# Kernel tuning notes

Measured on AMD Instinct MI355X. Metric: run time of the kernel, lower is better.

The kernel has to match this reference:

```python
import jax, jax.numpy as jnp
import numpy as np

N, DIM, DK, DV = 8192, 512, 128, 512


def setup_inputs() -> dict:
    key = jax.random.key(0)
    ks = jax.random.split(key, 6)
    return {
        "x": jax.random.normal(ks[0], (N, DIM), dtype=jnp.float32),
        "w_w": jax.random.normal(ks[1], (DK, DIM), dtype=jnp.float32) * (1.0 / np.sqrt(DIM)),
        "w_b": jax.random.normal(ks[2], (DK,), dtype=jnp.float32) * 0.01,
        "wv_w": jax.random.normal(ks[3], (DV, DIM), dtype=jnp.float32) * (1.0 / np.sqrt(DIM)),
        "wv_b": jax.random.normal(ks[4], (DV,), dtype=jnp.float32) * 0.01,
        "a": jax.random.normal(ks[5], (2 * DK,), dtype=jnp.float32),
    }


def reference(x, w_w, w_b, wv_w, wv_b, a):
    dk = w_b.shape[0]
    # eqx.nn.Linear: y = W @ x + b, applied per-row via vmap -> x @ W.T + b
    wx = x @ w_w.T + w_b                       # [n, dk]
    e_src = wx @ a[:dk]                        # [n], sum(wx_i * a1)
    e_dst = wx @ a[dk:]                        # [n], sum(wx_j * a2)
    logits = jax.nn.leaky_relu(e_src[:, None] + e_dst[None, :])  # [n, n]
    score = jax.nn.softmax(logits, axis=-1)    # row-wise softmax
    v = x @ wv_w.T + wv_b                      # [n, dv]
    return score @ v                           # [n, dv]
```

## Files before the change

### kernel.cpp

```cpp
#include <hip/hip_runtime.h>
#include <hip/hip_bf16.h>

#define N_   8192
#define DIM_ 512
#define DK_  128
#define DV_  512
#define L2E_ 1.44269504088896f
#define NCH_ 512
#define CHR_ 16

typedef short short8 __attribute__((ext_vector_type(8)));
typedef float f32x4  __attribute__((ext_vector_type(4)));

__device__ __forceinline__ float fexp2(float x) { return __builtin_amdgcn_exp2f(x); }

__device__ __forceinline__ ushort f2bf(float f) {
    union { float f; unsigned u; } v; v.f = f;
    unsigned u = v.u;
    return (ushort)((u + 0x7FFFu + ((u >> 16) & 1u)) >> 16);
}
__device__ __forceinline__ float bf2f(ushort u) { return __uint_as_float(((unsigned)u) << 16); }
__device__ __forceinline__ float decode_max(unsigned u) {
    return __uint_as_float((u & 0x80000000u) ? (u ^ 0x80000000u) : ~u);
}

__global__ __launch_bounds__(256) void prep_kernel(const float* __restrict__ w_w,
                            const float* __restrict__ w_b, const float* __restrict__ a,
                            const float* __restrict__ wv_w,
                            float* __restrict__ u1, float* __restrict__ u2,
                            float* __restrict__ scal, ushort* __restrict__ wvbf) {
    int bid = blockIdx.x, t = threadIdx.x;
    if (bid < 2) {
        int d = bid * 256 + t;
        float s1 = 0.f, s2 = 0.f;
        for (int k = 0; k < DK_; ++k) {
            float w = w_w[k * DIM_ + d];
            s1 += w * a[k];
            s2 += w * a[DK_ + k];
        }
        u1[d] = s1; u2[d] = s2;
        if (d == 0) { float c = 0.f; for (int k = 0; k < DK_; ++k) c += w_b[k] * a[k];        scal[0] = c; }
        if (d == 1) { float c = 0.f; for (int k = 0; k < DK_; ++k) c += w_b[k] * a[DK_ + k];  scal[1] = c; }
        if (d == 2) ((unsigned*)scal)[3] = 0u;
    } else {
        int idx = (bid - 2) * 2048 + t * 8;
        f32x4 lo = *(const f32x4*)(wv_w + idx);
        f32x4 hi = *(const f32x4*)(wv_w + idx + 4);
        short8 f;
#pragma unroll
        for (int e = 0; e < 4; ++e) { f[e] = (short)f2bf(lo[e]); f[e + 4] = (short)f2bf(hi[e]); }
        *(short8*)(wvbf + idx) = f;
    }
}

__global__ __launch_bounds__(256) void e_kernel(const float* __restrict__ x,
        const float* __restrict__ u1, const float* __restrict__ u2,
        const float* __restrict__ scal, float* __restrict__ e_src, float* __restrict__ e_dst,
        ushort* __restrict__ xbf, int* __restrict__ rank, int* __restrict__ ki,
        int* __restrict__ res) {
    int wid = threadIdx.x >> 6, lane = threadIdx.x & 63;
    int row = blockIdx.x * 4 + wid;
    const float* xr = x + (size_t)row * DIM_;
    int d0 = lane * 8;
    f32x4 xa = *(const f32x4*)(xr + d0);
    f32x4 xb = *(const f32x4*)(xr + d0 + 4);
    f32x4 ua = *(const f32x4*)(u1 + d0);
    f32x4 ub = *(const f32x4*)(u1 + d0 + 4);
    f32x4 va = *(const f32x4*)(u2 + d0);
    f32x4 vb = *(const f32x4*)(u2 + d0 + 4);
    short8 xv;
#pragma unroll
    for (int e = 0; e < 4; ++e) { xv[e] = (short)f2bf(xa[e]); xv[e + 4] = (short)f2bf(xb[e]); }
    *(short8*)(xbf + (size_t)row * DIM_ + d0) = xv;
    float s1 = 0.f, s2 = 0.f;
#pragma unroll
    for (int e = 0; e < 4; ++e) {
        s1 += xa[e] * ua[e] + xb[e] * ub[e];
        s2 += xa[e] * va[e] + xb[e] * vb[e];
    }
    for (int off = 32; off; off >>= 1) { s1 += __shfl_xor(s1, off); s2 += __shfl_xor(s2, off); }
    if (lane == 0) {
        e_src[row] = s1 + scal[0];
        e_dst[row] = s2 + scal[1];
    }
    if (lane == 1) rank[row] = 0;
    if (lane == 2) ki[row] = 0;
    if (lane == 3) res[row] = 0;
}

__global__ __launch_bounds__(256) void rankv_kernel(const float* __restrict__ e_dst,
        const float* __restrict__ e_src, int* __restrict__ rank, int* __restrict__ ki,
        int* __restrict__ res, float* __restrict__ scal,
        const ushort* __restrict__ xbf, const ushort* __restrict__ wvbf,
        const float* __restrict__ wv_b, ushort* __restrict__ V) {
    int bid = blockIdx.x, t = threadIdx.x;
    if (bid < 512) {
        __shared__ float ed[512];
        __shared__ float esl[512];
        __shared__ float red[4];
        int bx = bid & 31, by = bid >> 5;
        int rbase = by * 512;
        for (int q = t; q < 512; q += 256) { ed[q] = e_dst[rbase + q]; esl[q] = e_src[rbase + q]; }
        __syncthreads();
        if (bx == 0) {
            float m = fmaxf(ed[t], ed[t + 256]);
            for (int off = 32; off; off >>= 1) m = fmaxf(m, __shfl_xor(m, off));
            if ((t & 63) == 0) red[t >> 6] = m;
            __syncthreads();
            if (t == 0) {
                m = fmaxf(fmaxf(red[0], red[1]), fmaxf(red[2], red[3]));
                unsigned u = __float_as_uint(m);
                u ^= (unsigned)(((int)u >> 31)) | 0x80000000u;
                atomicMax(((unsigned*)scal) + 3, u);
            }
        }
        int j = bx * 256 + t;
        float kj = e_dst[j];
        float kei = -e_src[j];
        float kes = e_src[j];
        int cj = 0, ci = 0, ce = 0;
#pragma unroll 8
        for (int q = 0; q < 512; ++q) {
            float v = ed[q];
            float w = esl[q];
            int r = rbase + q;
            cj += (v < kj) || (v == kj && r < j);
            ci += (v < kei);
            ce += (w < kes) || (w == kes && r < j);
        }
        atomicAdd(rank + j, cj);
        atomicAdd(ki + j, ci);
        atomicAdd(res + j, ce);
    } else {
        int vb = bid - 512;
        int wid = t >> 6, lane = t & 63;
        int ln16 = lane & 15, kg = lane >> 4;
        int jb = (vb & 31) * 256 + wid * 64;
        int cb = (vb >> 5) * 64;
        f32x4 acc[4][4] = {};
        float bias[4];
#pragma unroll
        for (int ng = 0; ng < 4; ++ng) bias[ng] = wv_b[cb + ng * 16 + ln16];
        for (int k0 = 0; k0 < DIM_; k0 += 32) {
            int kk = k0 + kg * 8;
            short8 afr[4], bfr[4];
#pragma unroll
            for (int mg = 0; mg < 4; ++mg)
                afr[mg] = *(const short8*)(xbf + (size_t)(jb + mg * 16 + ln16) * DIM_ + kk);
#pragma unroll
            for (int ng = 0; ng < 4; ++ng)
                bfr[ng] = *(const short8*)(wvbf + (size_t)(cb + ng * 16 + ln16) * DIM_ + kk);
#pragma unroll
            for (int mg = 0; mg < 4; ++mg)
#pragma unroll
                for (int ng = 0; ng < 4; ++ng)
                    acc[mg][ng] = __builtin_amdgcn_mfma_f32_16x16x32_bf16(afr[mg], bfr[ng], acc[mg][ng], 0, 0, 0);
        }
#pragma unroll
        for (int mg = 0; mg < 4; ++mg)
#pragma unroll
            for (int ng = 0; ng < 4; ++ng)
#pragma unroll
                for (int r = 0; r < 4; ++r) {
                    int j = jb + mg * 16 + kg * 4 + r;
                    int c = cb + ng * 16 + ln16;
                    V[(size_t)j * DV_ + c] = f2bf(acc[mg][ng][r] + bias[ng]);
                }
    }
}

__global__ __launch_bounds__(256) void scatter_kernel(const float* __restrict__ e_dst,
        const int* __restrict__ rank, const int* __restrict__ res, const float* __restrict__ scal,
        int* __restrict__ perm, int* __restrict__ perm_es,
        float* __restrict__ Gs1, float* __restrict__ Gs2) {
    int j = blockIdx.x * 256 + threadIdx.x;
    float M = decode_max(((const unsigned*)scal)[3]);
    int rk = rank[j];
    float d = (e_dst[j] - M) * L2E_;
    perm[rk] = j;
    perm_es[res[j]] = j;
    Gs1[rk] = fexp2(d);
    Gs2[rk] = fexp2(0.01f * d);
}

__global__ __launch_bounds__(256) void p1_kernel(const ushort* __restrict__ V,
        const int* __restrict__ perm, const float* __restrict__ Gs1, const float* __restrict__ Gs2,
        float* __restrict__ C1, float* __restrict__ C2,
        float* __restrict__ C1z, float* __restrict__ C2z) {
    int ch = blockIdx.x >> 1, half = blockIdx.x & 1;
    int c = half * 256 + threadIdx.x;
    int k0 = ch * CHR_;
    int   jj[CHR_];
    float g1[CHR_], g2[CHR_], v[CHR_];
#pragma unroll
    for (int r = 0; r < CHR_; ++r) { jj[r] = perm[k0 + r]; g1[r] = Gs1[k0 + r]; g2[r] = Gs2[k0 + r]; }
#pragma unroll
    for (int r = 0; r < CHR_; ++r) v[r] = bf2f(V[(size_t)jj[r] * DV_ + c]);
    float a1 = 0.f, a2 = 0.f, z1 = 0.f, z2 = 0.f;
#pragma unroll
    for (int r = 0; r < CHR_; ++r) {
        a1 += g1[r] * v[r]; a2 += g2[r] * v[r];
        z1 += g1[r]; z2 += g2[r];
    }
    C1[ch * 512 + c] = a1; C2[ch * 512 + c] = a2;
    if (half == 0 && threadIdx.x == 0) { C1z[ch] = z1; C2z[ch] = z2; }
}

__global__ __launch_bounds__(256) void p2_kernel(const float* __restrict__ C1,
        const float* __restrict__ C2, const float* __restrict__ C1z, const float* __restrict__ C2z,
        float* __restrict__ pc2, float* __restrict__ sc1,
        float* __restrict__ pz2, float* __restrict__ sz1) {
    int b = blockIdx.x, t = threadIdx.x;
    if (b < 64) {
        int colL = t >> 5, s = t & 31;
        int c = b * 8 + colL;
        int base = s * 16;
        float v[16]; float seg = 0.f;
#pragma unroll
        for (int q = 0; q < 16; ++q) { v[q] = C2[(base + q) * 512 + c]; seg += v[q]; }
        float x = seg;
#pragma unroll
        for (int d = 1; d < 32; d <<= 1) { float y = __shfl_up(x, d, 32); if (s >= d) x += y; }
        float run = x - seg;
#pragma unroll
        for (int q = 0; q < 16; ++q) { pc2[(base + q) * 512 + c] = run; run += v[q]; }
        if (s == 31) pc2[NCH_ * 512 + c] = run;
    } else if (b < 128) {
        int colL = t >> 5, s = t & 31;
        int c = (b - 64) * 8 + colL;
        int base = s * 16;
        float v[16]; float seg = 0.f;
#pragma unroll
        for (int q = 0; q < 16; ++q) { v[q] = C1[(base + q) * 512 + c]; seg += v[q]; }
        float x = seg;
#pragma unroll
        for (int d = 1; d < 32; d <<= 1) { float y = __shfl_down(x, d, 32); if (s + d < 32) x += y; }
        float fwd = 0.f;
#pragma unroll
        for (int q = 0; q < 16; ++q) { sc1[(base + q) * 512 + c] = x - fwd; fwd += v[q]; }
        if (s == 31) sc1[NCH_ * 512 + c] = 0.f;
    } else {
        __shared__ float wt[4];
        bool pre = (b == 128);
        float v0 = pre ? C2z[t * 2] : C1z[t * 2];
        float v1 = pre ? C2z[t * 2 + 1] : C1z[t * 2 + 1];
        float seg = v0 + v1;
        int lane = t & 63, w = t >> 6;
        float x = seg;
        if (pre) {
#pragma unroll
            for (int d = 1; d < 64; d <<= 1) { float y = __shfl_up(x, d); if (lane >= d) x += y; }
            if (lane == 63) wt[w] = x;
        } else {
#pragma unroll
            for (int d = 1; d < 64; d <<= 1) { float y = __shfl_down(x, d); if (lane + d < 64) x += y; }
            if (lane == 0) wt[w] = x;
        }
        __syncthreads();
        float off = 0.f;
        if (pre) {
            for (int u = 0; u < w; ++u) off += wt[u];
            float run = off + (x - seg);
            pz2[t * 2] = run; run += v0; pz2[t * 2 + 1] = run;
            if (t == 255) pz2[NCH_] = off + x;
        } else {
            for (int u = w + 1; u < 4; ++u) off += wt[u];
            float S = off + x;
            sz1[t * 2] = S; sz1[t * 2 + 1] = S - v0;
            if (t == 255) sz1[NCH_] = 0.f;
        }
    }
}

__global__ __launch_bounds__(256) void p3_kernel(const ushort* __restrict__ V,
        const int* __restrict__ perm, const float* __restrict__ Gs1, const float* __restrict__ Gs2,
        const float* __restrict__ pc2, const float* __restrict__ sc1,
        const float* __restrict__ pz2, const float* __restrict__ sz1,
        unsigned* __restrict__ Pk, float* __restrict__ za, float* __restrict__ zs) {
    int ch = blockIdx.x >> 1, half = blockIdx.x & 1;
    int t = threadIdx.x;
    int c = half * 256 + t;
    int k0 = ch * CHR_;
    int   jj[CHR_];
    float g1[CHR_], g2[CHR_], v[CHR_];
#pragma unroll
    for (int r = 0; r < CHR_; ++r) { jj[r] = perm[k0 + r]; g1[r] = Gs1[k0 + r]; g2[r] = Gs2[k0 + r]; }
#pragma unroll
    for (int r = 0; r < CHR_; ++r) v[r] = bf2f(V[(size_t)jj[r] * DV_ + c]);
    float r2 = pc2[ch * 512 + c];
    float sc = sc1[ch * 512 + c];
    bool zown = (half == 0 && t == 0);
    float zp = 0.f, zsx = 0.f;
    if (zown) { zp = pz2[ch]; zsx = sz1[ch]; }
    float p1r = 0.f, z1p = 0.f;
#pragma unroll
    for (int r = 0; r < CHR_; ++r) {
        int k = k0 + r;
        Pk[(size_t)k * DV_ + c] = (unsigned)f2bf(r2) | ((unsigned)f2bf(sc - p1r) << 16);
        if (zown) { za[k] = zp; zs[k] = zsx - z1p; }
        r2  += g2[r] * v[r];  p1r += g1[r] * v[r];
        zp  += g2[r];         z1p += g1[r];
    }
    if (ch == NCH_ - 1) {
        Pk[(size_t)N_ * DV_ + c] = (unsigned)f2bf(pc2[NCH_ * 512 + c]) | ((unsigned)f2bf(0.f) << 16);
        if (zown) { za[N_] = pz2[NCH_]; zs[N_] = 0.f; }
    }
}

__global__ __launch_bounds__(256) void out_kernel(const float* __restrict__ e_src,
        const float* __restrict__ scal, const int* __restrict__ ki,
        const int* __restrict__ perm_es,
        const float* __restrict__ za, const float* __restrict__ zs,
        const unsigned* __restrict__ Pk, float* __restrict__ out) {
    int t = threadIdx.x;
    float M = decode_max(((const unsigned*)scal)[3]);
    int idx0 = blockIdx.x * 16;
    int c2 = t * 2;
#pragma unroll 2
    for (int q = 0; q < 16; ++q) {
        int i = perm_es[idx0 + q];
        float es = e_src[i];
        float tt = es + M;
        float m = fmaxf(tt, 0.01f * tt);
        float F1 = fexp2((tt - m) * L2E_);
        float F2 = fexp2((0.01f * tt - m) * L2E_);
        int lo = ki[i];
        float z = F2 * za[lo] + F1 * zs[lo];
        float rz = 1.0f / z;
        const unsigned* pt = Pk + (size_t)lo * DV_;
        unsigned w0 = pt[c2], w1 = pt[c2 + 1];
        float o0 = (F2 * bf2f((ushort)(w0 & 0xFFFFu)) + F1 * bf2f((ushort)(w0 >> 16))) * rz;
        float o1 = (F2 * bf2f((ushort)(w1 & 0xFFFFu)) + F1 * bf2f((ushort)(w1 >> 16))) * rz;
        out[(size_t)i * DV_ + c2]     = o0;
        out[(size_t)i * DV_ + c2 + 1] = o1;
    }
}

extern "C" void kernel_launch(void* const* d_in, const int* in_sizes, int n_in,
                              void* d_out, int out_size, void* d_ws, size_t ws_size,
                              hipStream_t stream) {
    const float* x    = (const float*)d_in[0];
    const float* w_w  = (const float*)d_in[1];
    const float* w_b  = (const float*)d_in[2];
    const float* wv_w = (const float*)d_in[3];
    const float* wv_b = (const float*)d_in[4];
    const float* a    = (const float*)d_in[5];
    float* out = (float*)d_out;
    char* ws = (char*)d_ws;

    ushort*   V    = (ushort*)(ws);
    ushort*   xbf  = (ushort*)(ws + 8388608);
    unsigned* Pk   = (unsigned*)(ws + 16777216);
    char*     sm   = ws + 35651584;
    float*  u1      = (float*)(sm);
    float*  u2      = (float*)(sm + 2048);
    float*  e_src   = (float*)(sm + 4096);
    float*  e_dst   = (float*)(sm + 36864);
    float*  scal    = (float*)(sm + 69632);
    float*  Gs1     = (float*)(sm + 69888);
    float*  Gs2     = (float*)(sm + 102656);
    float*  za      = (float*)(sm + 135424);
    float*  zs      = (float*)(sm + 168448);
    float*  C1      = (float*)(sm + 201472);
    float*  C2      = (float*)(sm + 1250048);
    float*  pc2     = (float*)(sm + 2298624);
    float*  sc1     = (float*)(sm + 3349248);
    float*  C1z     = (float*)(sm + 4399872);
    float*  C2z     = (float*)(sm + 4401920);
    float*  pz2     = (float*)(sm + 4403968);
    float*  sz1     = (float*)(sm + 4408064);
    int*    perm    = (int*)  (sm + 4412160);
    int*    rank    = (int*)  (sm + 4444928);
    int*    ki      = (int*)  (sm + 4477696);
    int*    res     = (int*)  (sm + 4510464);
    int*    perm_es = (int*)  (sm + 4543232);
    ushort* wvbf    = (ushort*)(sm + 4576000);

    hipLaunchKernelGGL(prep_kernel,    dim3(130),     dim3(256), 0, stream, w_w, w_b, a, wv_w, u1, u2, scal, wvbf);
    hipLaunchKernelGGL(e_kernel,       dim3(N_ / 4),  dim3(256), 0, stream, x, u1, u2, scal, e_src, e_dst, xbf, rank, ki, res);
    hipLaunchKernelGGL(rankv_kernel,   dim3(768),     dim3(256), 0, stream, e_dst, e_src, rank, ki, res, scal, xbf, wvbf, wv_b, V);
    hipLaunchKernelGGL(scatter_kernel, dim3(32),      dim3(256), 0, stream, e_dst, rank, res, scal, perm, perm_es, Gs1, Gs2);
    hipLaunchKernelGGL(p1_kernel,      dim3(1024),    dim3(256), 0, stream, V, perm, Gs1, Gs2, C1, C2, C1z, C2z);
    hipLaunchKernelGGL(p2_kernel,      dim3(130),     dim3(256), 0, stream, C1, C2, C1z, C2z, pc2, sc1, pz2, sz1);
    hipLaunchKernelGGL(p3_kernel,      dim3(1024),    dim3(256), 0, stream, V, perm, Gs1, Gs2, pc2, sc1, pz2, sz1, Pk, za, zs);
    hipLaunchKernelGGL(out_kernel,     dim3(N_ / 16), dim3(256), 0, stream, e_src, scal, ki, perm_es, za, zs, Pk, out);
}
```

Before: 88.89 us.

## Fuse local prefix pass into p1 and drop p3 by splitting scan offsets

The prefix-sum structure is split into chunk-local prefixes, written by p1 directly into Pk, plus chunk-level offsets from p2 that out_kernel adds at read time. This removes the p3 kernel, its second gather of V rows and its extra launch. In exchange out_kernel does two extra float2 reads of chunk offsets per row. Local prefixes stored in bf16 are now smaller values, which may change rounding behaviour.

```diff
diff --git a/kernel.cpp b/kernel.cpp
--- a/kernel.cpp
+++ b/kernel.cpp
@@ -11,6 +11,7 @@
 
 typedef short short8 __attribute__((ext_vector_type(8)));
 typedef float f32x4  __attribute__((ext_vector_type(4)));
+typedef float f32x2  __attribute__((ext_vector_type(2)));
 
 __device__ __forceinline__ float fexp2(float x) { return __builtin_amdgcn_exp2f(x); }
 
@@ -185,10 +186,12 @@
 
 __global__ __launch_bounds__(256) void p1_kernel(const ushort* __restrict__ V,
         const int* __restrict__ perm, const float* __restrict__ Gs1, const float* __restrict__ Gs2,
-        float* __restrict__ C1, float* __restrict__ C2,
-        float* __restrict__ C1z, float* __restrict__ C2z) {
+        unsigned* __restrict__ Pk, float* __restrict__ C1, float* __restrict__ C2,
+        float* __restrict__ C1z, float* __restrict__ C2z,
+        float* __restrict__ zl2, float* __restrict__ zl1) {
     int ch = blockIdx.x >> 1, half = blockIdx.x & 1;
-    int c = half * 256 + threadIdx.x;
+    int t = threadIdx.x;
+    int c = half * 256 + t;
     int k0 = ch * CHR_;
     int   jj[CHR_];
     float g1[CHR_], g2[CHR_], v[CHR_];
@@ -196,20 +199,38 @@
     for (int r = 0; r < CHR_; ++r) { jj[r] = perm[k0 + r]; g1[r] = Gs1[k0 + r]; g2[r] = Gs2[k0 + r]; }
 #pragma unroll
     for (int r = 0; r < CHR_; ++r) v[r] = bf2f(V[(size_t)jj[r] * DV_ + c]);
-    float a1 = 0.f, a2 = 0.f, z1 = 0.f, z2 = 0.f;
+    float t1 = 0.f, t2 = 0.f;
+#pragma unroll
+    for (int r = 0; r < CHR_; ++r) { t1 += g1[r] * v[r]; t2 += g2[r] * v[r]; }
+    float r2 = 0.f, p1r = 0.f;
 #pragma unroll
     for (int r = 0; r < CHR_; ++r) {
-        a1 += g1[r] * v[r]; a2 += g2[r] * v[r];
-        z1 += g1[r]; z2 += g2[r];
-    }
-    C1[ch * 512 + c] = a1; C2[ch * 512 + c] = a2;
-    if (half == 0 && threadIdx.x == 0) { C1z[ch] = z1; C2z[ch] = z2; }
+        Pk[(size_t)(k0 + r) * DV_ + c] = (unsigned)f2bf(r2) | ((unsigned)f2bf(t1 - p1r) << 16);
+        r2 += g2[r] * v[r]; p1r += g1[r] * v[r];
+    }
+    C1[ch * 512 + c] = t1; C2[ch * 512 + c] = t2;
+    if (half == 0 && t == 0) {
+        float z1t = 0.f, z2t = 0.f;
+#pragma unroll
+        for (int r = 0; r < CHR_; ++r) { z1t += g1[r]; z2t += g2[r]; }
+        C1z[ch] = z1t; C2z[ch] = z2t;
+        float zp2 = 0.f, zp1 = 0.f;
+#pragma unroll
+        for (int r = 0; r < CHR_; ++r) {
+            zl2[k0 + r] = zp2; zl1[k0 + r] = z1t - zp1;
+            zp2 += g2[r]; zp1 += g1[r];
+        }
+    }
+    if (ch == NCH_ - 1) {
+        Pk[(size_t)N_ * DV_ + c] = 0u;
+        if (half == 0 && t == 0) { zl2[N_] = 0.f; zl1[N_] = 0.f; }
+    }
 }
 
 __global__ __launch_bounds__(256) void p2_kernel(const float* __restrict__ C1,
         const float* __restrict__ C2, const float* __restrict__ C1z, const float* __restrict__ C2z,
-        float* __restrict__ pc2, float* __restrict__ sc1,
-        float* __restrict__ pz2, float* __restrict__ sz1) {
+        float* __restrict__ pc2, float* __restrict__ scs,
+        float* __restrict__ zc2, float* __restrict__ zc1) {
     int b = blockIdx.x, t = threadIdx.x;
     if (b < 64) {
         int colL = t >> 5, s = t & 31;
@@ -237,8 +258,8 @@
         for (int d = 1; d < 32; d <<= 1) { float y = __shfl_down(x, d, 32); if (s + d < 32) x += y; }
         float fwd = 0.f;
 #pragma unroll
-        for (int q = 0; q < 16; ++q) { sc1[(base + q) * 512 + c] = x - fwd; fwd += v[q]; }
-        if (s == 31) sc1[NCH_ * 512 + c] = 0.f;
+        for (int q = 0; q < 16; ++q) { fwd += v[q]; scs[(base + q) * 512 + c] = x - fwd; }
+        if (s == 31) scs[NCH_ * 512 + c] = 0.f;
     } else {
         __shared__ float wt[4];
         bool pre = (b == 128);
@@ -261,56 +282,24 @@
         if (pre) {
             for (int u = 0; u < w; ++u) off += wt[u];
             float run = off + (x - seg);
-            pz2[t * 2] = run; run += v0; pz2[t * 2 + 1] = run;
-            if (t == 255) pz2[NCH_] = off + x;
+            zc2[t * 2] = run; run += v0; zc2[t * 2 + 1] = run;
+            if (t == 255) zc2[NCH_] = off + x;
         } else {
             for (int u = w + 1; u < 4; ++u) off += wt[u];
             float S = off + x;
-            sz1[t * 2] = S; sz1[t * 2 + 1] = S - v0;
-            if (t == 255) sz1[NCH_] = 0.f;
-        }
-    }
-}
-
-__global__ __launch_bounds__(256) void p3_kernel(const ushort* __restrict__ V,
-        const int* __restrict__ perm, const float* __restrict__ Gs1, const float* __restrict__ Gs2,
-        const float* __restrict__ pc2, const float* __restrict__ sc1,
-        const float* __restrict__ pz2, const float* __restrict__ sz1,
-        unsigned* __restrict__ Pk, float* __restrict__ za, float* __restrict__ zs) {
-    int ch = blockIdx.x >> 1, half = blockIdx.x & 1;
-    int t = threadIdx.x;
-    int c = half * 256 + t;
-    int k0 = ch * CHR_;
-    int   jj[CHR_];
-    float g1[CHR_], g2[CHR_], v[CHR_];
-#pragma unroll
-    for (int r = 0; r < CHR_; ++r) { jj[r] = perm[k0 + r]; g1[r] = Gs1[k0 + r]; g2[r] = Gs2[k0 + r]; }
-#pragma unroll
-    for (int r = 0; r < CHR_; ++r) v[r] = bf2f(V[(size_t)jj[r] * DV_ + c]);
-    float r2 = pc2[ch * 512 + c];
-    float sc = sc1[ch * 512 + c];
-    bool zown = (half == 0 && t == 0);
-    float zp = 0.f, zsx = 0.f;
-    if (zown) { zp = pz2[ch]; zsx = sz1[ch]; }
-    float p1r = 0.f, z1p = 0.f;
-#pragma unroll
-    for (int r = 0; r < CHR_; ++r) {
-        int k = k0 + r;
-        Pk[(size_t)k * DV_ + c] = (unsigned)f2bf(r2) | ((unsigned)f2bf(sc - p1r) << 16);
-        if (zown) { za[k] = zp; zs[k] = zsx - z1p; }
-        r2  += g2[r] * v[r];  p1r += g1[r] * v[r];
-        zp  += g2[r];         z1p += g1[r];
-    }
-    if (ch == NCH_ - 1) {
-        Pk[(size_t)N_ * DV_ + c] = (unsigned)f2bf(pc2[NCH_ * 512 + c]) | ((unsigned)f2bf(0.f) << 16);
-        if (zown) { za[N_] = pz2[NCH_]; zs[N_] = 0.f; }
+            zc1[t * 2]     = S - v0;
+            zc1[t * 2 + 1] = S - v0 - v1;
+            if (t == 255) zc1[NCH_] = 0.f;
+        }
     }
 }
 
 __global__ __launch_bounds__(256) void out_kernel(const float* __restrict__ e_src,
         const float* __restrict__ scal, const int* __restrict__ ki,
         const int* __restrict__ perm_es,
-        const float* __restrict__ za, const float* __restrict__ zs,
+        const float* __restrict__ zl2, const float* __restrict__ zl1,
+        const float* __restrict__ zc2, const float* __restrict__ zc1,
+        const float* __restrict__ pc2, const float* __restrict__ scs,
         const unsigned* __restrict__ Pk, float* __restrict__ out) {
     int t = threadIdx.x;
     float M = decode_max(((const unsigned*)scal)[3]);
@@ -325,12 +314,15 @@
         float F1 = fexp2((tt - m) * L2E_);
         float F2 = fexp2((0.01f * tt - m) * L2E_);
         int lo = ki[i];
-        float z = F2 * za[lo] + F1 * zs[lo];
+        int ch = lo >> 4;
+        float z = F2 * (zc2[ch] + zl2[lo]) + F1 * (zc1[ch] + zl1[lo]);
         float rz = 1.0f / z;
         const unsigned* pt = Pk + (size_t)lo * DV_;
         unsigned w0 = pt[c2], w1 = pt[c2 + 1];
-        float o0 = (F2 * bf2f((ushort)(w0 & 0xFFFFu)) + F1 * bf2f((ushort)(w0 >> 16))) * rz;
-        float o1 = (F2 * bf2f((ushort)(w1 & 0xFFFFu)) + F1 * bf2f((ushort)(w1 >> 16))) * rz;
+        f32x2 cp = *(const f32x2*)(pc2 + ch * 512 + c2);
+        f32x2 cs = *(const f32x2*)(scs + ch * 512 + c2);
+        float o0 = (F2 * (cp[0] + bf2f((ushort)(w0 & 0xFFFFu))) + F1 * (cs[0] + bf2f((ushort)(w0 >> 16)))) * rz;
+        float o1 = (F2 * (cp[1] + bf2f((ushort)(w1 & 0xFFFFu))) + F1 * (cs[1] + bf2f((ushort)(w1 >> 16)))) * rz;
         out[(size_t)i * DV_ + c2]     = o0;
         out[(size_t)i * DV_ + c2 + 1] = o1;
     }
@@ -359,29 +351,28 @@
     float*  scal    = (float*)(sm + 69632);
     float*  Gs1     = (float*)(sm + 69888);
     float*  Gs2     = (float*)(sm + 102656);
-    float*  za      = (float*)(sm + 135424);
-    float*  zs      = (float*)(sm + 168448);
-    float*  C1      = (float*)(sm + 201472);
-    float*  C2      = (float*)(sm + 1250048);
-    float*  pc2     = (float*)(sm + 2298624);
-    float*  sc1     = (float*)(sm + 3349248);
-    float*  C1z     = (float*)(sm + 4399872);
-    float*  C2z     = (float*)(sm + 4401920);
-    float*  pz2     = (float*)(sm + 4403968);
-    float*  sz1     = (float*)(sm + 4408064);
-    int*    perm    = (int*)  (sm + 4412160);
-    int*    rank    = (int*)  (sm + 4444928);
-    int*    ki      = (int*)  (sm + 4477696);
-    int*    res     = (int*)  (sm + 4510464);
-    int*    perm_es = (int*)  (sm + 4543232);
-    ushort* wvbf    = (ushort*)(sm + 4576000);
+    float*  C1      = (float*)(sm + 135424);
+    float*  C2      = (float*)(sm + 1184000);
+    float*  pc2     = (float*)(sm + 2232576);
+    float*  scs     = (float*)(sm + 3284224);
+    float*  C1z     = (float*)(sm + 4335872);
+    float*  C2z     = (float*)(sm + 4337920);
+    float*  zl2     = (float*)(sm + 4339968);
+    float*  zl1     = (float*)(sm + 4372992);
+    float*  zc2     = (float*)(sm + 4406016);
+    float*  zc1     = (float*)(sm + 4410112);
+    int*    perm    = (int*)  (sm + 4414208);
+    int*    rank    = (int*)  (sm + 4446976);
+    int*    ki      = (int*)  (sm + 4479744);
+    int*    res     = (int*)  (sm + 4512512);
+    int*    perm_es = (int*)  (sm + 4545280);
+    ushort* wvbf    = (ushort*)(sm + 4578048);
 
     hipLaunchKernelGGL(prep_kernel,    dim3(130),     dim3(256), 0, stream, w_w, w_b, a, wv_w, u1, u2, scal, wvbf);
     hipLaunchKernelGGL(e_kernel,       dim3(N_ / 4),  dim3(256), 0, stream, x, u1, u2, scal, e_src, e_dst, xbf, rank, ki, res);
     hipLaunchKernelGGL(rankv_kernel,   dim3(768),     dim3(256), 0, stream, e_dst, e_src, rank, ki, res, scal, xbf, wvbf, wv_b, V);
     hipLaunchKernelGGL(scatter_kernel, dim3(32),      dim3(256), 0, stream, e_dst, rank, res, scal, perm, perm_es, Gs1, Gs2);
-    hipLaunchKernelGGL(p1_kernel,      dim3(1024),    dim3(256), 0, stream, V, perm, Gs1, Gs2, C1, C2, C1z, C2z);
-    hipLaunchKernelGGL(p2_kernel,      dim3(130),     dim3(256), 0, stream, C1, C2, C1z, C2z, pc2, sc1, pz2, sz1);
-    hipLaunchKernelGGL(p3_kernel,      dim3(1024),    dim3(256), 0, stream, V, perm, Gs1, Gs2, pc2, sc1, pz2, sz1, Pk, za, zs);
-    hipLaunchKernelGGL(out_kernel,     dim3(N_ / 16), dim3(256), 0, stream, e_src, scal, ki, perm_es, za, zs, Pk, out);
-}
+    hipLaunchKernelGGL(p1_kernel,      dim3(1024),    dim3(256), 0, stream, V, perm, Gs1, Gs2, Pk, C1, C2, C1z, C2z, zl2, zl1);
+    hipLaunchKernelGGL(p2_kernel,      dim3(130),     dim3(256), 0, stream, C1, C2, C1z, C2z, pc2, scs, zc2, zc1);
+    hipLaunchKernelGGL(out_kernel,     dim3(N_ / 16), dim3(256), 0, stream, e_src, scal, ki, perm_es, zl2, zl1, zc2, zc1, pc2, scs, Pk, out);
+}
```

Result: faster. 85.42 us (-3.9%).
